# Optimization experiments

Hardware: AMD Instinct MI355X
Metric: run time of the kernel (lower is better)

## Reference

```python
import jax, jax.numpy as jnp
import numpy as np


def setup_inputs() -> dict:
    key = jax.random.key(0)
    B, C, L = 32, 8, 4096
    x = jax.random.normal(key, (B, C, L), dtype=jnp.float32)
    return {"k": 64, "input": x}


def reference(k, input):
    # input: [B, C, L]; build sliding windows [B, C, L-k+1, k] via gather
    L = input.shape[2]
    idx = jnp.arange(L - k + 1)[:, None] + jnp.arange(k)[None, :]  # [L-k+1, k]
    windows = input[:, :, idx]  # [B, C, L-k+1, k]
    logp = jax.nn.log_softmax(windows, axis=-1)
    # sum(softmax * log_softmax) = sum(exp(logp) * logp)
    return jnp.sum(jnp.exp(logp) * logp, axis=-1)  # [B, C, L-k+1]
```

## Files before the change

kernel.cpp:

```cpp
#include <hip/hip_runtime.h>
#include <math.h>


#define KWIN 64
#define LROW 4096
#define NWIN 4033
#define BLOCKS_PER_ROW 4
#define OUT_PER_BLOCK 1024
#define THREADS 256
#define WPT 4

__global__ __launch_bounds__(THREADS)
void entropy_win_kernel(const float* __restrict__ x, float* __restrict__ out) {
    __shared__ __align__(16) float E[OUT_PER_BLOCK + KWIN];
    __shared__ __align__(16) float F[OUT_PER_BLOCK + KWIN];
    __shared__ __align__(16) float O[OUT_PER_BLOCK];

    const int bid  = blockIdx.x;
    const int row  = bid / BLOCKS_PER_ROW;
    const int q    = bid % BLOCKS_PER_ROW;
    const int out0 = q * OUT_PER_BLOCK;
    const int tid  = threadIdx.x;

    int nload = LROW - out0;
    if (nload > OUT_PER_BLOCK + KWIN - 1) nload = OUT_PER_BLOCK + KWIN - 1;

    int nout = NWIN - out0;
    if (nout > OUT_PER_BLOCK) nout = OUT_PER_BLOCK;

    const float* __restrict__ xr = x + row * LROW + out0;

    for (int i = tid; i < nload; i += THREADS) {
        float v = xr[i];
        float e = __expf(v);
        E[i] = e;
        F[i] = e * v;
    }
    __syncthreads();

    const int base = tid * WPT;
    if (base < nout) {
        const float4* E4 = (const float4*)(E + base);
        const float4* F4 = (const float4*)(F + base);
        float4 s4 = make_float4(0.f, 0.f, 0.f, 0.f);
        float4 t4 = make_float4(0.f, 0.f, 0.f, 0.f);
#pragma unroll
        for (int j = 0; j < KWIN / 4; ++j) {
            float4 e = E4[j];
            float4 f = F4[j];
            s4.x += e.x; s4.y += e.y; s4.z += e.z; s4.w += e.w;
            t4.x += f.x; t4.y += f.y; t4.z += f.z; t4.w += f.w;
        }
        float S = (s4.x + s4.y) + (s4.z + s4.w);
        float T = (t4.x + t4.y) + (t4.z + t4.w);

#pragma unroll
        for (int w = 0; w < WPT; ++w) {
            int g = base + w;
            if (g < nout) {
                O[g] = T / S - __logf(S);
            }
            if (w < WPT - 1) {
                S += E[base + KWIN + w] - E[base + w];
                T += F[base + KWIN + w] - F[base + w];
            }
        }
    }
    __syncthreads();

    float* __restrict__ orow = out + row * NWIN + out0;
    for (int i = tid; i < nout; i += THREADS) {
        orow[i] = O[i];
    }
}

extern "C" void kernel_launch(void* const* d_in, const int* in_sizes, int n_in,
                              void* d_out, int out_size, void* d_ws, size_t ws_size,
                              hipStream_t stream) {
    const float* x = (const float*)d_in[1];
    float* out = (float*)d_out;
    (void)d_in; (void)in_sizes; (void)n_in; (void)out_size; (void)d_ws; (void)ws_size;

    dim3 grid(256 * BLOCKS_PER_ROW);
    dim3 block(THREADS);
    entropy_win_kernel<<<grid, block, 0, stream>>>(x, out);
}
```

Before: 10.26 us.

## Replace per-thread window sums with block-wide prefix scan differences

```diff
diff --git a/kernel.cpp b/kernel.cpp
--- a/kernel.cpp
+++ b/kernel.cpp
@@ -8,69 +8,85 @@
 #define BLOCKS_PER_ROW 4
 #define OUT_PER_BLOCK 1024
 #define THREADS 256
-#define WPT 4
+#define CHUNK 5
+#define SCAN_N (THREADS * CHUNK)
 
 __global__ __launch_bounds__(THREADS)
 void entropy_win_kernel(const float* __restrict__ x, float* __restrict__ out) {
-    __shared__ __align__(16) float E[OUT_PER_BLOCK + KWIN];
-    __shared__ __align__(16) float F[OUT_PER_BLOCK + KWIN];
-    __shared__ __align__(16) float O[OUT_PER_BLOCK];
+    __shared__ __align__(16) float PE[SCAN_N];
+    __shared__ __align__(16) float PF[SCAN_N];
+    __shared__ float wsumE[4], wsumF[4];
 
     const int bid  = blockIdx.x;
     const int row  = bid / BLOCKS_PER_ROW;
     const int q    = bid % BLOCKS_PER_ROW;
     const int out0 = q * OUT_PER_BLOCK;
     const int tid  = threadIdx.x;
+    const int lane = tid & 63;
+    const int wid  = tid >> 6;
 
     int nload = LROW - out0;
     if (nload > OUT_PER_BLOCK + KWIN - 1) nload = OUT_PER_BLOCK + KWIN - 1;
-
     int nout = NWIN - out0;
     if (nout > OUT_PER_BLOCK) nout = OUT_PER_BLOCK;
 
     const float* __restrict__ xr = x + row * LROW + out0;
 
-    for (int i = tid; i < nload; i += THREADS) {
-        float v = xr[i];
-        float e = __expf(v);
-        E[i] = e;
-        F[i] = e * v;
+    float e[CHUNK], f[CHUNK];
+    const int c0 = CHUNK * tid;
+    float se = 0.f, sf = 0.f;
+#pragma unroll
+    for (int i = 0; i < CHUNK; ++i) {
+        int g = c0 + i;
+        float ee = 0.f, ff = 0.f;
+        if (g < nload) {
+            float v = xr[g];
+            ee = __expf(v);
+            ff = ee * v;
+        }
+        e[i] = ee;
+        f[i] = ff;
+        se += ee;
+        sf += ff;
     }
+
+    float ise = se, isf = sf;
+#pragma unroll
+    for (int d = 1; d < 64; d <<= 1) {
+        float ue = __shfl_up(ise, d, 64);
+        float uf = __shfl_up(isf, d, 64);
+        if (lane >= d) { ise += ue; isf += uf; }
+    }
+    if (lane == 63) { wsumE[wid] = ise; wsumF[wid] = isf; }
     __syncthreads();
 
-    const int base = tid * WPT;
-    if (base < nout) {
-        const float4* E4 = (const float4*)(E + base);
-        const float4* F4 = (const float4*)(F + base);
-        float4 s4 = make_float4(0.f, 0.f, 0.f, 0.f);
-        float4 t4 = make_float4(0.f, 0.f, 0.f, 0.f);
+    float offE = 0.f, offF = 0.f;
 #pragma unroll
-        for (int j = 0; j < KWIN / 4; ++j) {
-            float4 e = E4[j];
-            float4 f = F4[j];
-            s4.x += e.x; s4.y += e.y; s4.z += e.z; s4.w += e.w;
-            t4.x += f.x; t4.y += f.y; t4.z += f.z; t4.w += f.w;
-        }
-        float S = (s4.x + s4.y) + (s4.z + s4.w);
-        float T = (t4.x + t4.y) + (t4.z + t4.w);
+    for (int wv = 0; wv < 3; ++wv) {
+        if (wv < wid) { offE += wsumE[wv]; offF += wsumF[wv]; }
+    }
+
+    float pe = offE + (ise - se);
+    float pf = offF + (isf - sf);
 
 #pragma unroll
-        for (int w = 0; w < WPT; ++w) {
-            int g = base + w;
-            if (g < nout) {
-                O[g] = T / S - __logf(S);
-            }
-            if (w < WPT - 1) {
-                S += E[base + KWIN + w] - E[base + w];
-                T += F[base + KWIN + w] - F[base + w];
-            }
-        }
+    for (int i = 0; i < CHUNK; ++i) {
+        PE[c0 + i] = pe;
+        PF[c0 + i] = pf;
+        pe += e[i];
+        pf += f[i];
     }
     __syncthreads();
 
     float* __restrict__ orow = out + row * NWIN + out0;
-    for (int i = tid; i < nout; i += THREADS) {
-        orow[i] = O[i];
+#pragma unroll
+    for (int w = 0; w < 4; ++w) {
+        int g = tid + w * THREADS;
+        if (g < nout) {
+            float S = PE[g + KWIN] - PE[g];
+            float T = PF[g + KWIN] - PF[g];
+            orow[g] = T / S - __logf(S);
+        }
     }
 }
 
@@ -79,7 +95,7 @@
                               hipStream_t stream) {
     const float* x = (const float*)d_in[1];
     float* out = (float*)d_out;
-    (void)d_in; (void)in_sizes; (void)n_in; (void)out_size; (void)d_ws; (void)ws_size;
+    (void)in_sizes; (void)n_in; (void)out_size; (void)d_ws; (void)ws_size;
 
     dim3 grid(256 * BLOCKS_PER_ROW);
     dim3 block(THREADS);
```

Measured after the change: 10.43 us. About the same (+1.7%).
